# Kernel tuning notes

Hardware: AMD Instinct MI355X
Metric: run time of the kernel (lower is better)

The kernel has to match this reference:

```python
import jax, jax.numpy as jnp
import numpy as np

N, L, C, H, W, HEAD = 16, 256, 512, 32, 32, 16

def setup_inputs() -> dict:
    key = jax.random.key(0)
    ks = jax.random.split(key, 8)
    s = 0.02  # weight init scale
    return {
        "feature": jax.random.normal(ks[0], (N, C, H, W), jnp.float32),
        "token": jax.random.normal(ks[1], (N, L, C), jnp.float32),
        "wq": jax.random.normal(ks[2], (C, C), jnp.float32) * s,
        "bq": jax.random.normal(ks[3], (C,), jnp.float32) * s,
        "wk": jax.random.normal(ks[4], (C, C), jnp.float32) * s,
        "bk": jax.random.normal(ks[5], (C,), jnp.float32) * s,
        "wv": jax.random.normal(ks[6], (C, C), jnp.float32) * s,
        "bv": jax.random.normal(ks[7], (C,), jnp.float32) * s,
    }

def reference(feature, token, wq, bq, wk, bk, wv, bv):
    n, c, hgt, wid = feature.shape
    h = HEAD
    d = c // h
    l = token.shape[1]
    scale = jnp.asarray(np.sqrt(c / h), feature.dtype)
    tok = token.transpose(0, 2, 1)  # (N, C, L)
    # 1x1 conv projections == per-position GEMMs
    v = (jnp.einsum('ncl,dc->ndl', tok, wv) + bv[None, :, None]).reshape(n, h, d, l)
    k = (jnp.einsum('ncl,dc->ndl', tok, wk) + bk[None, :, None]).reshape(n, h, d, l)
    q = (jnp.einsum('nchw,dc->ndhw', feature, wq) + bq[None, :, None, None])
    q = q.reshape(n, h, d, hgt * wid).transpose(0, 1, 3, 2)  # (N, h, HW, d)
    scores = jnp.einsum('nhqd,nhdl->nhql', q, k) / scale  # (N, h, HW, L)
    coef = jax.nn.softmax(scores, axis=-1)
    proj = jnp.einsum('nhdl,nhql->nhdq', v, coef)  # (N, h, d, HW)
    return feature + proj.reshape(n, c, hgt, wid)
```

## Files before the change

### kernel.cpp

```cpp
#include <hip/hip_runtime.h>
#include <hip/hip_bf16.h>

#define N_ 16
#define L_ 256
#define C_ 512
#define HW_ 1024
#define HEADS_ 16
#define DH_ 32

typedef unsigned short u16;
typedef unsigned int u32;
typedef __attribute__((ext_vector_type(8))) short short8_t;
typedef __attribute__((ext_vector_type(4))) float f32x4;
typedef __attribute__((ext_vector_type(2))) unsigned int u32x2;

__device__ __forceinline__ u16 f2bs(float f) {
    union { float f; u32 i; } x; x.f = f;
    u32 r = x.i + 0x7fffu + ((x.i >> 16) & 1u);
    return (u16)(r >> 16);
}
__device__ __forceinline__ u32 cvt_pk_bf16(float lo, float hi) {
    u32 r;
    asm("v_cvt_pk_bf16_f32 %0, %1, %2" : "=v"(r) : "v"(lo), "v"(hi));
    return r;
}

__global__ __launch_bounds__(256) void prep_kernel(
    const float* __restrict__ token, const float* __restrict__ wq,
    const float* __restrict__ wk, const float* __restrict__ wv,
    u16* __restrict__ tokb, u16* __restrict__ wqb,
    u16* __restrict__ wkb, u16* __restrict__ wvb)
{
    const int idx = blockIdx.x * 256 + threadIdx.x;
    const float* s; u16* d; int off;
    if (idx < 524288)            { s = token; d = tokb; off = idx; }
    else if (idx < 524288+65536) { s = wq; d = wqb; off = idx - 524288; }
    else if (idx < 524288+131072){ s = wk; d = wkb; off = idx - 524288 - 65536; }
    else                         { s = wv; d = wvb; off = idx - 524288 - 131072; }
    float4 v = ((const float4*)s)[off];
    ushort4 w;
    w.x = f2bs(v.x); w.y = f2bs(v.y); w.z = f2bs(v.z); w.w = f2bs(v.w);
    ((ushort4*)d)[off] = w;
}

__global__ __launch_bounds__(256) void gemm_qf_kernel(
    const float* __restrict__ feature, const u16* __restrict__ Wb,
    const float* __restrict__ bias, u16* __restrict__ Out)
{
    __shared__ __align__(16) unsigned char smem[16384];
    u16* As = (u16*)smem;
    u16* Bs = (u16*)(smem + 8192);

    const int t = threadIdx.x;
    const int m0 = blockIdx.x * 64, n0 = blockIdx.y * 64;
    const int n = m0 >> 10, pos0 = m0 & (HW_ - 1);
    const int lane = t & 63, wid = t >> 6;
    const int i16 = lane & 15, g = lane >> 4;
    const int wm = wid >> 1, wn = wid & 1;
    const int row_a = t >> 3, c8 = t & 7;
    const int cst = t >> 2, pq = t & 3;

    f32x4 acc[2][2] = {{{0.f,0.f,0.f,0.f},{0.f,0.f,0.f,0.f}},
                       {{0.f,0.f,0.f,0.f},{0.f,0.f,0.f,0.f}}};

    for (int c0 = 0; c0 < C_; c0 += 64) {
        __syncthreads();
        #pragma unroll
        for (int r = 0; r < 2; ++r) {
            const int m = row_a + r * 32;
            *(short8_t*)&As[m * 64 + ((c8 ^ (m & 7)) << 3)] =
                *(const short8_t*)&Wb[(size_t)(n0 + m) * C_ + c0 + c8 * 8];
        }
        #pragma unroll
        for (int j = 0; j < 4; ++j) {
            const int pos = j * 16 + pq * 4;
            float4 v = *(const float4*)&feature[
                ((size_t)n * C_ + c0 + cst) * HW_ + pos0 + pos];
            ushort4 w;
            w.x = f2bs(v.x); w.y = f2bs(v.y); w.z = f2bs(v.z); w.w = f2bs(v.w);
            *(ushort4*)&Bs[(cst >> 2) * 256 + j * 64 + (cst & 3) * 16 + pq * 4] = w;
        }
        __syncthreads();
        #pragma unroll
        for (int ks = 0; ks < 2; ++ks) {
            short8_t a[2];
            #pragma unroll
            for (int mt = 0; mt < 2; ++mt) {
                const int m = wm * 32 + mt * 16 + i16;
                a[mt] = *(const short8_t*)&As[m * 64 + ((((ks << 2) | g) ^ (m & 7)) << 3)];
            }
            short8_t b[2];
            #pragma unroll
            for (int nt = 0; nt < 2; ++nt) {
                const int pb = wn * 2 + nt;
                const u32 vaddr = 8192 +
                    (u32)(ks * 32 + g * 8 + pb) * 128 + (u32)i16 * 2;
                u32x2 lo, hi;
                asm volatile("ds_read_b64_tr_b16 %0, %1"
                             : "=v"(lo) : "v"(vaddr));
                asm volatile("ds_read_b64_tr_b16 %0, %1 offset:512"
                             : "=v"(hi) : "v"(vaddr));
                union { u32 w[4]; short8_t v; } pk;
                pk.w[0] = lo[0]; pk.w[1] = lo[1];
                pk.w[2] = hi[0]; pk.w[3] = hi[1];
                b[nt] = pk.v;
            }
            asm volatile("s_waitcnt lgkmcnt(0)" ::: "memory");
            __builtin_amdgcn_sched_barrier(0);
            #pragma unroll
            for (int mt = 0; mt < 2; ++mt)
                #pragma unroll
                for (int nt = 0; nt < 2; ++nt)
                    acc[mt][nt] = __builtin_amdgcn_mfma_f32_16x16x32_bf16(
                        a[mt], b[nt], acc[mt][nt], 0, 0, 0);
        }
    }
    #pragma unroll
    for (int mt = 0; mt < 2; ++mt) {
        const int dbase = wm * 32 + mt * 16 + g * 4;
        float4 b4 = *(const float4*)&bias[n0 + dbase];
        const float bb[4] = {b4.x, b4.y, b4.z, b4.w};
        #pragma unroll
        for (int nt = 0; nt < 2; ++nt) {
            const int pos = wn * 32 + nt * 16 + i16;
            ushort4 w;
            w.x = f2bs(acc[mt][nt][0] + bb[0]);
            w.y = f2bs(acc[mt][nt][1] + bb[1]);
            w.z = f2bs(acc[mt][nt][2] + bb[2]);
            w.w = f2bs(acc[mt][nt][3] + bb[3]);
            *(ushort4*)&Out[(size_t)(m0 + pos) * C_ + n0 + dbase] = w;
        }
    }
}

__global__ __launch_bounds__(256) void gemm_kv_kernel(
    const u16* __restrict__ A, const u16* __restrict__ Wkb,
    const u16* __restrict__ Wvb, const float* __restrict__ bk,
    const float* __restrict__ bv, u16* __restrict__ Kout, u16* __restrict__ Vt)
{
    __shared__ __align__(16) unsigned char smem[24576];
    u16* As  = (u16*)smem;
    u16* Bks = (u16*)(smem + 8192);
    u16* Bvs = (u16*)(smem + 16384);
    u16 (*LTo)[72] = (u16(*)[72])smem;

    const int t = threadIdx.x;
    const int m0 = blockIdx.x * 64, n0 = blockIdx.y * 64;
    const int lane = t & 63, wid = t >> 6;
    const int i16 = lane & 15, g = lane >> 4;
    const int wm = wid >> 1, wn = wid & 1;
    const int row_a = t >> 3, c8 = t & 7;

    f32x4 ak[2][2] = {{{0.f,0.f,0.f,0.f},{0.f,0.f,0.f,0.f}},
                      {{0.f,0.f,0.f,0.f},{0.f,0.f,0.f,0.f}}};
    f32x4 av[2][2] = {{{0.f,0.f,0.f,0.f},{0.f,0.f,0.f,0.f}},
                      {{0.f,0.f,0.f,0.f},{0.f,0.f,0.f,0.f}}};
    const float bk0 = bk[n0 + wn * 32 + i16];
    const float bk1 = bk[n0 + wn * 32 + 16 + i16];
    const float bv0 = bv[n0 + wn * 32 + i16];
    const float bv1 = bv[n0 + wn * 32 + 16 + i16];

    for (int c0 = 0; c0 < C_; c0 += 64) {
        __syncthreads();
        #pragma unroll
        for (int r = 0; r < 2; ++r) {
            const int m = row_a + r * 32;
            const int sw = m * 64 + ((c8 ^ (m & 7)) << 3);
            *(short8_t*)&As[sw]  = *(const short8_t*)&A[(size_t)(m0 + m) * C_ + c0 + c8 * 8];
            *(short8_t*)&Bks[sw] = *(const short8_t*)&Wkb[(size_t)(n0 + m) * C_ + c0 + c8 * 8];
            *(short8_t*)&Bvs[sw] = *(const short8_t*)&Wvb[(size_t)(n0 + m) * C_ + c0 + c8 * 8];
        }
        __syncthreads();
        #pragma unroll
        for (int ks = 0; ks < 2; ++ks) {
            short8_t a[2], bbk[2], bbv[2];
            #pragma unroll
            for (int mt = 0; mt < 2; ++mt) {
                const int m = wm * 32 + mt * 16 + i16;
                a[mt] = *(const short8_t*)&As[m * 64 + ((((ks << 2) | g) ^ (m & 7)) << 3)];
            }
            #pragma unroll
            for (int nt = 0; nt < 2; ++nt) {
                const int d = wn * 32 + nt * 16 + i16;
                const int sw = d * 64 + ((((ks << 2) | g) ^ (d & 7)) << 3);
                bbk[nt] = *(const short8_t*)&Bks[sw];
                bbv[nt] = *(const short8_t*)&Bvs[sw];
            }
            #pragma unroll
            for (int mt = 0; mt < 2; ++mt)
                #pragma unroll
                for (int nt = 0; nt < 2; ++nt) {
                    ak[mt][nt] = __builtin_amdgcn_mfma_f32_16x16x32_bf16(
                        a[mt], bbk[nt], ak[mt][nt], 0, 0, 0);
                    av[mt][nt] = __builtin_amdgcn_mfma_f32_16x16x32_bf16(
                        a[mt], bbv[nt], av[mt][nt], 0, 0, 0);
                }
        }
    }
    const int nb = m0 >> 8, l0 = m0 & 255;
    const size_t vtbase = (size_t)nb * C_ * L_;
    #pragma unroll
    for (int mt = 0; mt < 2; ++mt)
        #pragma unroll
        for (int nt = 0; nt < 2; ++nt) {
            const int d = n0 + wn * 32 + nt * 16 + i16;
            const float bb = nt ? bv1 : bv0;
            ushort4 w;
            w.x = f2bs(av[mt][nt][0] + bb);
            w.y = f2bs(av[mt][nt][1] + bb);
            w.z = f2bs(av[mt][nt][2] + bb);
            w.w = f2bs(av[mt][nt][3] + bb);
            const int l = l0 + wm * 32 + mt * 16 + g * 4;
            *(ushort4*)&Vt[vtbase + (size_t)d * L_ + l] = w;
        }
    __syncthreads();
    #pragma unroll
    for (int mt = 0; mt < 2; ++mt)
        #pragma unroll
        for (int nt = 0; nt < 2; ++nt) {
            const float bb = nt ? bk1 : bk0;
            #pragma unroll
            for (int r = 0; r < 4; ++r)
                LTo[wm * 32 + mt * 16 + g * 4 + r][wn * 32 + nt * 16 + i16] =
                    f2bs(ak[mt][nt][r] + bb);
        }
    __syncthreads();
    #pragma unroll
    for (int rep = 0; rep < 2; ++rep) {
        const int m = (t >> 3) + rep * 32;
        const int cs = (t & 7) * 8;
        *(short8_t*)&Kout[(size_t)(m0 + m) * C_ + n0 + cs] = *(short8_t*)&LTo[m][cs];
    }
}

__global__ __launch_bounds__(256) void attn_kernel(
    const u16* __restrict__ Qws, const u16* __restrict__ Kws,
    const u16* __restrict__ Vws, const float* __restrict__ feature,
    float* __restrict__ out)
{
    __shared__ __align__(16) unsigned char smem[32768];

    const int t = threadIdx.x;
    const int wid = t >> 6, lane = t & 63;
    const int i16 = lane & 15, g = lane >> 4;
    const int pt = blockIdx.x, h = blockIdx.y, n = blockIdx.z;
    const int pos0 = pt * 64;
    const size_t qbase = ((size_t)n * HW_ + pos0) * C_ + h * DH_;
    const size_t kbase = ((size_t)n * L_) * C_ + h * DH_;
    const size_t vbase = (size_t)n * C_ * L_ + (size_t)h * DH_ * L_;

    const int q = wid * 16 + i16;

    short8_t bq = *(const short8_t*)&Qws[qbase + (size_t)q * C_ + g * 8];

    #pragma unroll
    for (int p = 0; p < 4; ++p) {
        const int kr = wid * 64 + p * 16 + (lane >> 2);
        const int kg = (lane & 3) ^ ((lane >> 3) & 3);
        const u16* ksrc = Kws + kbase + (size_t)kr * C_ + kg * 8;
        __builtin_amdgcn_global_load_lds(
            (const __attribute__((address_space(1))) void*)ksrc,
            (__attribute__((address_space(3))) void*)(smem + wid * 4096 + p * 1024),
            16, 0, 0);
        const int vd = wid * 8 + p * 2 + (lane >> 5);
        const u16* vsrc = Vws + vbase + (size_t)vd * L_ + ((lane & 31) ^ (vd & 7)) * 8;
        __builtin_amdgcn_global_load_lds(
            (const __attribute__((address_space(1))) void*)vsrc,
            (__attribute__((address_space(3))) void*)(smem + 16384 + wid * 4096 + p * 1024),
            16, 0, 0);
    }
    __syncthreads();

    const int kgr = g ^ ((i16 >> 1) & 3);
    f32x4 s[16];
    #pragma unroll
    for (int nf = 0; nf < 16; ++nf) {
        short8_t a = *(const short8_t*)(smem + (nf * 16 + i16) * 64 + kgr * 16);
        f32x4 z = {0.f, 0.f, 0.f, 0.f};
        s[nf] = __builtin_amdgcn_mfma_f32_16x16x32_bf16(a, bq, z, 0, 0, 0);
    }

    float mm[16], sm[16];
    #pragma unroll
    for (int nf = 0; nf < 16; ++nf)
        mm[nf] = fmaxf(fmaxf(s[nf][0], s[nf][1]), fmaxf(s[nf][2], s[nf][3]));
    #pragma unroll
    for (int st = 8; st >= 1; st >>= 1)
        #pragma unroll
        for (int i = 0; i < 8; ++i)
            if (i < st) mm[i] = fmaxf(mm[i], mm[i + st]);
    float m = mm[0];
    m = fmaxf(m, __shfl_xor(m, 16));
    m = fmaxf(m, __shfl_xor(m, 32));

    const float K2 = 0.25506288f;
    #pragma unroll
    for (int nf = 0; nf < 16; ++nf) {
        #pragma unroll
        for (int r = 0; r < 4; ++r) s[nf][r] = exp2f((s[nf][r] - m) * K2);
        sm[nf] = (s[nf][0] + s[nf][1]) + (s[nf][2] + s[nf][3]);
    }
    #pragma unroll
    for (int st = 8; st >= 1; st >>= 1)
        #pragma unroll
        for (int i = 0; i < 8; ++i)
            if (i < st) sm[i] += sm[i + st];
    float ssum = sm[0];
    ssum += __shfl_xor(ssum, 16);
    ssum += __shfl_xor(ssum, 32);
    const float pinv = 1.0f / ssum;

    __syncthreads();

    f32x4 o0 = {0.f, 0.f, 0.f, 0.f}, o1 = {0.f, 0.f, 0.f, 0.f};
    const int e7 = i16 & 7;

    #pragma unroll
    for (int hb = 0; hb < 2; ++hb) {
        #pragma unroll
        for (int nfp = 0; nfp < 8; ++nfp) {
            const int nf = hb * 8 + nfp;
            #pragma unroll
            for (int w = 0; w < 2; ++w) {
                u32 pw = cvt_pk_bf16(s[nf][2 * w] * pinv, s[nf][2 * w + 1] * pinv);
                const int gran = (nfp * 2 + (g >> 1)) ^ e7;
                *(u32*)(smem + q * 256 + gran * 16 + ((g & 1) * 2 + w) * 4) = pw;
            }
        }
        __syncthreads();
        #pragma unroll
        for (int ks = 0; ks < 4; ++ks) {
            short8_t pb = *(const short8_t*)(smem + q * 256 + (((ks * 4 + g) ^ e7) * 16));
            const int vg = (((hb * 4 + ks) * 4 + g) ^ e7) * 16;
            short8_t va0 = *(const short8_t*)(smem + 16384 + i16 * 512 + vg);
            short8_t va1 = *(const short8_t*)(smem + 16384 + (16 + i16) * 512 + vg);
            o0 = __builtin_amdgcn_mfma_f32_16x16x32_bf16(va0, pb, o0, 0, 0, 0);
            o1 = __builtin_amdgcn_mfma_f32_16x16x32_bf16(va1, pb, o1, 0, 0, 0);
        }
        if (hb == 0) __syncthreads();
    }

    const size_t obase = ((size_t)n * C_ + h * DH_) * HW_ + pos0 + q;
    #pragma unroll
    for (int r = 0; r < 4; ++r) {
        const size_t oa = obase + (size_t)(g * 4 + r) * HW_;
        out[oa] = feature[oa] + o0[r];
        const size_t ob = obase + (size_t)(16 + g * 4 + r) * HW_;
        out[ob] = feature[ob] + o1[r];
    }
}

extern "C" void kernel_launch(void* const* d_in, const int* in_sizes, int n_in,
                              void* d_out, int out_size, void* d_ws, size_t ws_size,
                              hipStream_t stream)
{
    const float* feature = (const float*)d_in[0];
    const float* token   = (const float*)d_in[1];
    const float* wq      = (const float*)d_in[2];
    const float* bq      = (const float*)d_in[3];
    const float* wk      = (const float*)d_in[4];
    const float* bk      = (const float*)d_in[5];
    const float* wv      = (const float*)d_in[6];
    const float* bv      = (const float*)d_in[7];
    float* out = (float*)d_out;

    u16* Qws = (u16*)d_ws;
    u16* Kws = Qws + (size_t)N_ * HW_ * C_;
    u16* Vws = Kws + (size_t)N_ * L_ * C_;

    char* ob = (char*)d_out;
    u16* tokb = (u16*)(ob + (16u << 20));
    u16* wqb  = (u16*)(ob + (20u << 20));
    u16* wkb  = (u16*)(ob + (20u << 20) + 524288);
    u16* wvb  = (u16*)(ob + (20u << 20) + 1048576);

    prep_kernel<<<dim3(2816), 256, 0, stream>>>(token, wq, wk, wv,
                                                tokb, wqb, wkb, wvb);
    gemm_qf_kernel<<<dim3(256, 8), 256, 0, stream>>>(feature, wqb, bq, Qws);
    gemm_kv_kernel<<<dim3(64, 8), 256, 0, stream>>>(tokb, wkb, wvb, bk, bv,
                                                    Kws, Vws);
    attn_kernel<<<dim3(16, 16, 16), 256, 0, stream>>>(Qws, Kws, Vws, feature, out);
}
```

Baseline: 78.96 us.

## Fuse bf16 prep and Q/KV projection GEMMs into one proj kernel

Drops the separate fp32-to-bf16 prep kernel and the two projection GEMM launches, replacing them with one kernel whose blocks split into a K/V branch and a Q branch. Each branch converts fp32 token and weight tiles to bf16 inline while staging them into shared memory. The Q branch also reorders the feature tile load and preloads both k-steps of fragments before the MFMAs. This removes two launches and the intermediate bf16 round trip through global memory, at the cost of converting the weights again in every block and running a larger, divergent kernel.

```diff
diff --git a/kernel.cpp b/kernel.cpp
--- a/kernel.cpp
+++ b/kernel.cpp
@@ -24,212 +24,205 @@
     asm("v_cvt_pk_bf16_f32 %0, %1, %2" : "=v"(r) : "v"(lo), "v"(hi));
     return r;
 }
-
-__global__ __launch_bounds__(256) void prep_kernel(
-    const float* __restrict__ token, const float* __restrict__ wq,
-    const float* __restrict__ wk, const float* __restrict__ wv,
-    u16* __restrict__ tokb, u16* __restrict__ wqb,
-    u16* __restrict__ wkb, u16* __restrict__ wvb)
+__device__ __forceinline__ void cvt8(const float* __restrict__ src, void* dst) {
+    float4 lo = *(const float4*)src;
+    float4 hi = *(const float4*)(src + 4);
+    union { u32 w[4]; short8_t v; } pk;
+    pk.w[0] = cvt_pk_bf16(lo.x, lo.y);
+    pk.w[1] = cvt_pk_bf16(lo.z, lo.w);
+    pk.w[2] = cvt_pk_bf16(hi.x, hi.y);
+    pk.w[3] = cvt_pk_bf16(hi.z, hi.w);
+    *(short8_t*)dst = pk.v;
+}
+
+__global__ __launch_bounds__(256) void proj_kernel(
+    const float* __restrict__ feature, const float* __restrict__ token,
+    const float* __restrict__ wq, const float* __restrict__ bq,
+    const float* __restrict__ wk, const float* __restrict__ bk,
+    const float* __restrict__ wv, const float* __restrict__ bv,
+    u16* __restrict__ Qout, u16* __restrict__ Kout, u16* __restrict__ Vt)
 {
-    const int idx = blockIdx.x * 256 + threadIdx.x;
-    const float* s; u16* d; int off;
-    if (idx < 524288)            { s = token; d = tokb; off = idx; }
-    else if (idx < 524288+65536) { s = wq; d = wqb; off = idx - 524288; }
-    else if (idx < 524288+131072){ s = wk; d = wkb; off = idx - 524288 - 65536; }
-    else                         { s = wv; d = wvb; off = idx - 524288 - 131072; }
-    float4 v = ((const float4*)s)[off];
-    ushort4 w;
-    w.x = f2bs(v.x); w.y = f2bs(v.y); w.z = f2bs(v.z); w.w = f2bs(v.w);
-    ((ushort4*)d)[off] = w;
-}
-
-__global__ __launch_bounds__(256) void gemm_qf_kernel(
-    const float* __restrict__ feature, const u16* __restrict__ Wb,
-    const float* __restrict__ bias, u16* __restrict__ Out)
-{
-    __shared__ __align__(16) unsigned char smem[16384];
-    u16* As = (u16*)smem;
-    u16* Bs = (u16*)(smem + 8192);
+    __shared__ __align__(16) unsigned char smem[24576];
 
     const int t = threadIdx.x;
-    const int m0 = blockIdx.x * 64, n0 = blockIdx.y * 64;
-    const int n = m0 >> 10, pos0 = m0 & (HW_ - 1);
     const int lane = t & 63, wid = t >> 6;
     const int i16 = lane & 15, g = lane >> 4;
     const int wm = wid >> 1, wn = wid & 1;
-    const int row_a = t >> 3, c8 = t & 7;
-    const int cst = t >> 2, pq = t & 3;
-
-    f32x4 acc[2][2] = {{{0.f,0.f,0.f,0.f},{0.f,0.f,0.f,0.f}},
-                       {{0.f,0.f,0.f,0.f},{0.f,0.f,0.f,0.f}}};
-
-    for (int c0 = 0; c0 < C_; c0 += 64) {
+
+    if (blockIdx.x < 512) {
+        u16* As  = (u16*)smem;
+        u16* Bks = (u16*)(smem + 8192);
+        u16* Bvs = (u16*)(smem + 16384);
+        u16 (*LTo)[72] = (u16(*)[72])smem;
+
+        const int m0 = (blockIdx.x & 63) * 64, n0 = (blockIdx.x >> 6) * 64;
+        const int row_a = t >> 3, c8 = t & 7;
+
+        f32x4 ak[2][2] = {{{0.f,0.f,0.f,0.f},{0.f,0.f,0.f,0.f}},
+                          {{0.f,0.f,0.f,0.f},{0.f,0.f,0.f,0.f}}};
+        f32x4 av[2][2] = {{{0.f,0.f,0.f,0.f},{0.f,0.f,0.f,0.f}},
+                          {{0.f,0.f,0.f,0.f},{0.f,0.f,0.f,0.f}}};
+        const float bk0 = bk[n0 + wn * 32 + i16];
+        const float bk1 = bk[n0 + wn * 32 + 16 + i16];
+        const float bv0 = bv[n0 + wn * 32 + i16];
+        const float bv1 = bv[n0 + wn * 32 + 16 + i16];
+
+        for (int c0 = 0; c0 < C_; c0 += 64) {
+            __syncthreads();
+            #pragma unroll
+            for (int r = 0; r < 2; ++r) {
+                const int m = row_a + r * 32;
+                const int sw = m * 64 + ((c8 ^ (m & 7)) << 3);
+                cvt8(&token[(size_t)(m0 + m) * C_ + c0 + c8 * 8], &As[sw]);
+                cvt8(&wk[(size_t)(n0 + m) * C_ + c0 + c8 * 8], &Bks[sw]);
+                cvt8(&wv[(size_t)(n0 + m) * C_ + c0 + c8 * 8], &Bvs[sw]);
+            }
+            __syncthreads();
+            #pragma unroll
+            for (int ks = 0; ks < 2; ++ks) {
+                short8_t a[2], bbk[2], bbv[2];
+                #pragma unroll
+                for (int mt = 0; mt < 2; ++mt) {
+                    const int m = wm * 32 + mt * 16 + i16;
+                    a[mt] = *(const short8_t*)&As[m * 64 + ((((ks << 2) | g) ^ (m & 7)) << 3)];
+                }
+                #pragma unroll
+                for (int nt = 0; nt < 2; ++nt) {
+                    const int d = wn * 32 + nt * 16 + i16;
+                    const int sw = d * 64 + ((((ks << 2) | g) ^ (d & 7)) << 3);
+                    bbk[nt] = *(const short8_t*)&Bks[sw];
+                    bbv[nt] = *(const short8_t*)&Bvs[sw];
+                }
+                #pragma unroll
+                for (int mt = 0; mt < 2; ++mt)
+                    #pragma unroll
+                    for (int nt = 0; nt < 2; ++nt) {
+                        ak[mt][nt] = __builtin_amdgcn_mfma_f32_16x16x32_bf16(
+                            a[mt], bbk[nt], ak[mt][nt], 0, 0, 0);
+                        av[mt][nt] = __builtin_amdgcn_mfma_f32_16x16x32_bf16(
+                            a[mt], bbv[nt], av[mt][nt], 0, 0, 0);
+                    }
+            }
+        }
+        const int nb = m0 >> 8, l0 = m0 & 255;
+        const size_t vtbase = (size_t)nb * C_ * L_;
+        #pragma unroll
+        for (int mt = 0; mt < 2; ++mt)
+            #pragma unroll
+            for (int nt = 0; nt < 2; ++nt) {
+                const int d = n0 + wn * 32 + nt * 16 + i16;
+                const float bb = nt ? bv1 : bv0;
+                ushort4 w;
+                w.x = f2bs(av[mt][nt][0] + bb);
+                w.y = f2bs(av[mt][nt][1] + bb);
+                w.z = f2bs(av[mt][nt][2] + bb);
+                w.w = f2bs(av[mt][nt][3] + bb);
+                const int l = l0 + wm * 32 + mt * 16 + g * 4;
+                *(ushort4*)&Vt[vtbase + (size_t)d * L_ + l] = w;
+            }
         __syncthreads();
         #pragma unroll
-        for (int r = 0; r < 2; ++r) {
-            const int m = row_a + r * 32;
-            *(short8_t*)&As[m * 64 + ((c8 ^ (m & 7)) << 3)] =
-                *(const short8_t*)&Wb[(size_t)(n0 + m) * C_ + c0 + c8 * 8];
-        }
-        #pragma unroll
-        for (int j = 0; j < 4; ++j) {
-            const int pos = j * 16 + pq * 4;
-            float4 v = *(const float4*)&feature[
-                ((size_t)n * C_ + c0 + cst) * HW_ + pos0 + pos];
-            ushort4 w;
-            w.x = f2bs(v.x); w.y = f2bs(v.y); w.z = f2bs(v.z); w.w = f2bs(v.w);
-            *(ushort4*)&Bs[(cst >> 2) * 256 + j * 64 + (cst & 3) * 16 + pq * 4] = w;
-        }
+        for (int mt = 0; mt < 2; ++mt)
+            #pragma unroll
+            for (int nt = 0; nt < 2; ++nt) {
+                const float bb = nt ? bk1 : bk0;
+                #pragma unroll
+                for (int r = 0; r < 4; ++r)
+                    LTo[wm * 32 + mt * 16 + g * 4 + r][wn * 32 + nt * 16 + i16] =
+                        f2bs(ak[mt][nt][r] + bb);
+            }
         __syncthreads();
         #pragma unroll
-        for (int ks = 0; ks < 2; ++ks) {
-            short8_t a[2];
-            #pragma unroll
-            for (int mt = 0; mt < 2; ++mt) {
-                const int m = wm * 32 + mt * 16 + i16;
-                a[mt] = *(const short8_t*)&As[m * 64 + ((((ks << 2) | g) ^ (m & 7)) << 3)];
-            }
-            short8_t b[2];
-            #pragma unroll
-            for (int nt = 0; nt < 2; ++nt) {
-                const int pb = wn * 2 + nt;
-                const u32 vaddr = 8192 +
-                    (u32)(ks * 32 + g * 8 + pb) * 128 + (u32)i16 * 2;
-                u32x2 lo, hi;
-                asm volatile("ds_read_b64_tr_b16 %0, %1"
-                             : "=v"(lo) : "v"(vaddr));
-                asm volatile("ds_read_b64_tr_b16 %0, %1 offset:512"
-                             : "=v"(hi) : "v"(vaddr));
-                union { u32 w[4]; short8_t v; } pk;
-                pk.w[0] = lo[0]; pk.w[1] = lo[1];
-                pk.w[2] = hi[0]; pk.w[3] = hi[1];
-                b[nt] = pk.v;
-            }
+        for (int rep = 0; rep < 2; ++rep) {
+            const int m = (t >> 3) + rep * 32;
+            const int cs = (t & 7) * 8;
+            *(short8_t*)&Kout[(size_t)(m0 + m) * C_ + n0 + cs] = *(short8_t*)&LTo[m][cs];
+        }
+    } else {
+        u16* As = (u16*)smem;
+        u16* Bs = (u16*)(smem + 8192);
+
+        const int bid = blockIdx.x - 512;
+        const int m0 = (bid & 255) * 64, n0 = (bid >> 8) * 64;
+        const int n = m0 >> 10, pos0 = m0 & (HW_ - 1);
+        const int row_a = t >> 3, c8 = t & 7;
+
+        f32x4 acc[2][2] = {{{0.f,0.f,0.f,0.f},{0.f,0.f,0.f,0.f}},
+                           {{0.f,0.f,0.f,0.f},{0.f,0.f,0.f,0.f}}};
+
+        for (int c0 = 0; c0 < C_; c0 += 64) {
+            __syncthreads();
+            #pragma unroll
+            for (int r = 0; r < 2; ++r) {
+                const int m = row_a + r * 32;
+                cvt8(&wq[(size_t)(n0 + m) * C_ + c0 + c8 * 8],
+                     &As[m * 64 + ((c8 ^ (m & 7)) << 3)]);
+            }
+            #pragma unroll
+            for (int ps = 0; ps < 4; ++ps) {
+                const int row = ps * 16 + (t >> 4);
+                const int px = (t & 15) * 4;
+                float4 v = *(const float4*)&feature[
+                    ((size_t)n * C_ + c0 + row) * HW_ + pos0 + px];
+                ushort4 w;
+                w.x = f2bs(v.x); w.y = f2bs(v.y);
+                w.z = f2bs(v.z); w.w = f2bs(v.w);
+                *(ushort4*)&Bs[(row >> 2) * 256 + (px >> 4) * 64 +
+                               (row & 3) * 16 + (px & 15)] = w;
+            }
+            __syncthreads();
+            short8_t a2[2][2], b2[2][2];
+            #pragma unroll
+            for (int ks = 0; ks < 2; ++ks)
+                #pragma unroll
+                for (int mt = 0; mt < 2; ++mt) {
+                    const int m = wm * 32 + mt * 16 + i16;
+                    a2[ks][mt] = *(const short8_t*)&As[m * 64 + ((((ks << 2) | g) ^ (m & 7)) << 3)];
+                }
+            #pragma unroll
+            for (int ks = 0; ks < 2; ++ks)
+                #pragma unroll
+                for (int nt = 0; nt < 2; ++nt) {
+                    const int pb = wn * 2 + nt;
+                    const u32 vaddr = 8192 +
+                        (u32)(ks * 32 + g * 8 + pb) * 128 + (u32)i16 * 2;
+                    u32x2 lo, hi;
+                    asm volatile("ds_read_b64_tr_b16 %0, %1"
+                                 : "=v"(lo) : "v"(vaddr));
+                    asm volatile("ds_read_b64_tr_b16 %0, %1 offset:512"
+                                 : "=v"(hi) : "v"(vaddr));
+                    union { u32 w[4]; short8_t v; } pk;
+                    pk.w[0] = lo[0]; pk.w[1] = lo[1];
+                    pk.w[2] = hi[0]; pk.w[3] = hi[1];
+                    b2[ks][nt] = pk.v;
+                }
             asm volatile("s_waitcnt lgkmcnt(0)" ::: "memory");
             __builtin_amdgcn_sched_barrier(0);
             #pragma unroll
-            for (int mt = 0; mt < 2; ++mt)
-                #pragma unroll
-                for (int nt = 0; nt < 2; ++nt)
-                    acc[mt][nt] = __builtin_amdgcn_mfma_f32_16x16x32_bf16(
-                        a[mt], b[nt], acc[mt][nt], 0, 0, 0);
-        }
-    }
-    #pragma unroll
-    for (int mt = 0; mt < 2; ++mt) {
-        const int dbase = wm * 32 + mt * 16 + g * 4;
-        float4 b4 = *(const float4*)&bias[n0 + dbase];
-        const float bb[4] = {b4.x, b4.y, b4.z, b4.w};
-        #pragma unroll
-        for (int nt = 0; nt < 2; ++nt) {
-            const int pos = wn * 32 + nt * 16 + i16;
-            ushort4 w;
-            w.x = f2bs(acc[mt][nt][0] + bb[0]);
-            w.y = f2bs(acc[mt][nt][1] + bb[1]);
-            w.z = f2bs(acc[mt][nt][2] + bb[2]);
-            w.w = f2bs(acc[mt][nt][3] + bb[3]);
-            *(ushort4*)&Out[(size_t)(m0 + pos) * C_ + n0 + dbase] = w;
-        }
-    }
-}
-
-__global__ __launch_bounds__(256) void gemm_kv_kernel(
-    const u16* __restrict__ A, const u16* __restrict__ Wkb,
-    const u16* __restrict__ Wvb, const float* __restrict__ bk,
-    const float* __restrict__ bv, u16* __restrict__ Kout, u16* __restrict__ Vt)
-{
-    __shared__ __align__(16) unsigned char smem[24576];
-    u16* As  = (u16*)smem;
-    u16* Bks = (u16*)(smem + 8192);
-    u16* Bvs = (u16*)(smem + 16384);
-    u16 (*LTo)[72] = (u16(*)[72])smem;
-
-    const int t = threadIdx.x;
-    const int m0 = blockIdx.x * 64, n0 = blockIdx.y * 64;
-    const int lane = t & 63, wid = t >> 6;
-    const int i16 = lane & 15, g = lane >> 4;
-    const int wm = wid >> 1, wn = wid & 1;
-    const int row_a = t >> 3, c8 = t & 7;
-
-    f32x4 ak[2][2] = {{{0.f,0.f,0.f,0.f},{0.f,0.f,0.f,0.f}},
-                      {{0.f,0.f,0.f,0.f},{0.f,0.f,0.f,0.f}}};
-    f32x4 av[2][2] = {{{0.f,0.f,0.f,0.f},{0.f,0.f,0.f,0.f}},
-                      {{0.f,0.f,0.f,0.f},{0.f,0.f,0.f,0.f}}};
-    const float bk0 = bk[n0 + wn * 32 + i16];
-    const float bk1 = bk[n0 + wn * 32 + 16 + i16];
-    const float bv0 = bv[n0 + wn * 32 + i16];
-    const float bv1 = bv[n0 + wn * 32 + 16 + i16];
-
-    for (int c0 = 0; c0 < C_; c0 += 64) {
-        __syncthreads();
-        #pragma unroll
-        for (int r = 0; r < 2; ++r) {
-            const int m = row_a + r * 32;
-            const int sw = m * 64 + ((c8 ^ (m & 7)) << 3);
-            *(short8_t*)&As[sw]  = *(const short8_t*)&A[(size_t)(m0 + m) * C_ + c0 + c8 * 8];
-            *(short8_t*)&Bks[sw] = *(const short8_t*)&Wkb[(size_t)(n0 + m) * C_ + c0 + c8 * 8];
-            *(short8_t*)&Bvs[sw] = *(const short8_t*)&Wvb[(size_t)(n0 + m) * C_ + c0 + c8 * 8];
-        }
-        __syncthreads();
-        #pragma unroll
-        for (int ks = 0; ks < 2; ++ks) {
-            short8_t a[2], bbk[2], bbv[2];
-            #pragma unroll
-            for (int mt = 0; mt < 2; ++mt) {
-                const int m = wm * 32 + mt * 16 + i16;
-                a[mt] = *(const short8_t*)&As[m * 64 + ((((ks << 2) | g) ^ (m & 7)) << 3)];
-            }
+            for (int ks = 0; ks < 2; ++ks)
+                #pragma unroll
+                for (int mt = 0; mt < 2; ++mt)
+                    #pragma unroll
+                    for (int nt = 0; nt < 2; ++nt)
+                        acc[mt][nt] = __builtin_amdgcn_mfma_f32_16x16x32_bf16(
+                            a2[ks][mt], b2[ks][nt], acc[mt][nt], 0, 0, 0);
+        }
+        #pragma unroll
+        for (int mt = 0; mt < 2; ++mt) {
+            const int dbase = wm * 32 + mt * 16 + g * 4;
+            float4 b4 = *(const float4*)&bq[n0 + dbase];
+            const float bb[4] = {b4.x, b4.y, b4.z, b4.w};
             #pragma unroll
             for (int nt = 0; nt < 2; ++nt) {
-                const int d = wn * 32 + nt * 16 + i16;
-                const int sw = d * 64 + ((((ks << 2) | g) ^ (d & 7)) << 3);
-                bbk[nt] = *(const short8_t*)&Bks[sw];
-                bbv[nt] = *(const short8_t*)&Bvs[sw];
-            }
-            #pragma unroll
-            for (int mt = 0; mt < 2; ++mt)
-                #pragma unroll
-                for (int nt = 0; nt < 2; ++nt) {
-                    ak[mt][nt] = __builtin_amdgcn_mfma_f32_16x16x32_bf16(
-                        a[mt], bbk[nt], ak[mt][nt], 0, 0, 0);
-                    av[mt][nt] = __builtin_amdgcn_mfma_f32_16x16x32_bf16(
-                        a[mt], bbv[nt], av[mt][nt], 0, 0, 0);
-                }
-        }
-    }
-    const int nb = m0 >> 8, l0 = m0 & 255;
-    const size_t vtbase = (size_t)nb * C_ * L_;
-    #pragma unroll
-    for (int mt = 0; mt < 2; ++mt)
-        #pragma unroll
-        for (int nt = 0; nt < 2; ++nt) {
-            const int d = n0 + wn * 32 + nt * 16 + i16;
-            const float bb = nt ? bv1 : bv0;
-            ushort4 w;
-            w.x = f2bs(av[mt][nt][0] + bb);
-            w.y = f2bs(av[mt][nt][1] + bb);
-            w.z = f2bs(av[mt][nt][2] + bb);
-            w.w = f2bs(av[mt][nt][3] + bb);
-            const int l = l0 + wm * 32 + mt * 16 + g * 4;
-            *(ushort4*)&Vt[vtbase + (size_t)d * L_ + l] = w;
-        }
-    __syncthreads();
-    #pragma unroll
-    for (int mt = 0; mt < 2; ++mt)
-        #pragma unroll
-        for (int nt = 0; nt < 2; ++nt) {
-            const float bb = nt ? bk1 : bk0;
-            #pragma unroll
-            for (int r = 0; r < 4; ++r)
-                LTo[wm * 32 + mt * 16 + g * 4 + r][wn * 32 + nt * 16 + i16] =
-                    f2bs(ak[mt][nt][r] + bb);
-        }
-    __syncthreads();
-    #pragma unroll
-    for (int rep = 0; rep < 2; ++rep) {
-        const int m = (t >> 3) + rep * 32;
-        const int cs = (t & 7) * 8;
-        *(short8_t*)&Kout[(size_t)(m0 + m) * C_ + n0 + cs] = *(short8_t*)&LTo[m][cs];
+                const int pos = wn * 32 + nt * 16 + i16;
+                ushort4 w;
+                w.x = f2bs(acc[mt][nt][0] + bb[0]);
+                w.y = f2bs(acc[mt][nt][1] + bb[1]);
+                w.z = f2bs(acc[mt][nt][2] + bb[2]);
+                w.w = f2bs(acc[mt][nt][3] + bb[3]);
+                *(ushort4*)&Qout[(size_t)(m0 + pos) * C_ + n0 + dbase] = w;
+            }
+        }
     }
 }
 
@@ -255,8 +248,8 @@
 
     #pragma unroll
     for (int p = 0; p < 4; ++p) {
+        const int kg = (lane & 3) ^ ((lane >> 3) & 3);
         const int kr = wid * 64 + p * 16 + (lane >> 2);
-        const int kg = (lane & 3) ^ ((lane >> 3) & 3);
         const u16* ksrc = Kws + kbase + (size_t)kr * C_ + kg * 8;
         __builtin_amdgcn_global_load_lds(
             (const __attribute__((address_space(1))) void*)ksrc,
@@ -368,16 +361,8 @@
     u16* Kws = Qws + (size_t)N_ * HW_ * C_;
     u16* Vws = Kws + (size_t)N_ * L_ * C_;
 
-    char* ob = (char*)d_out;
-    u16* tokb = (u16*)(ob + (16u << 20));
-    u16* wqb  = (u16*)(ob + (20u << 20));
-    u16* wkb  = (u16*)(ob + (20u << 20) + 524288);
-    u16* wvb  = (u16*)(ob + (20u << 20) + 1048576);
-
-    prep_kernel<<<dim3(2816), 256, 0, stream>>>(token, wq, wk, wv,
-                                                tokb, wqb, wkb, wvb);
-    gemm_qf_kernel<<<dim3(256, 8), 256, 0, stream>>>(feature, wqb, bq, Qws);
-    gemm_kv_kernel<<<dim3(64, 8), 256, 0, stream>>>(tokb, wkb, wvb, bk, bv,
-                                                    Kws, Vws);
+    proj_kernel<<<dim3(2560), 256, 0, stream>>>(feature, token, wq, bq,
+                                                wk, bk, wv, bv,
+                                                Qws, Kws, Vws);
     attn_kernel<<<dim3(16, 16, 16), 256, 0, stream>>>(Qws, Kws, Vws, feature, out);
 }
```

New measurement: 79.37 us. About the same (+0.5%).

## Merge Q and KV projection GEMMs into one launch with larger tiles

Applied to the files above, without the earlier changes.

Combines the separate Q-projection and K/V-projection GEMM kernels into a single proj_kernel. Blocks below 256 compute K/V and the rest compute Q, which removes a launch and lets both GEMMs share the GPU at once. Tiles grow to 128x64 for KV and 128x128 for Q, operand tiles are loaded with global_load_lds direct-to-LDS copies, and block indices are remapped so consecutive tiles stay on the same XCD. The larger tiles raise register and LDS use (36 KB), which may lower occupancy, and the mixed block roles can leave the load unbalanced.

```diff
diff --git a/kernel.cpp b/kernel.cpp
--- a/kernel.cpp
+++ b/kernel.cpp
@@ -24,6 +24,18 @@
     asm("v_cvt_pk_bf16_f32 %0, %1, %2" : "=v"(r) : "v"(lo), "v"(hi));
     return r;
 }
+__device__ __forceinline__ void cvt8(const float* __restrict__ src, void* dst) {
+    float4 lo = *(const float4*)src;
+    float4 hi = *(const float4*)(src + 4);
+    union { u32 w[4]; short8_t v; } pk;
+    pk.w[0] = cvt_pk_bf16(lo.x, lo.y);
+    pk.w[1] = cvt_pk_bf16(lo.z, lo.w);
+    pk.w[2] = cvt_pk_bf16(hi.x, hi.y);
+    pk.w[3] = cvt_pk_bf16(hi.z, hi.w);
+    *(short8_t*)dst = pk.v;
+}
+#define AS1(p) (const __attribute__((address_space(1))) void*)(p)
+#define AS3(p) (__attribute__((address_space(3))) void*)(p)
 
 __global__ __launch_bounds__(256) void prep_kernel(
     const float* __restrict__ token, const float* __restrict__ wq,
@@ -43,193 +55,215 @@
     ((ushort4*)d)[off] = w;
 }
 
-__global__ __launch_bounds__(256) void gemm_qf_kernel(
-    const float* __restrict__ feature, const u16* __restrict__ Wb,
-    const float* __restrict__ bias, u16* __restrict__ Out)
+__global__ __launch_bounds__(256) void proj_kernel(
+    const float* __restrict__ feature,
+    const u16* __restrict__ tokb, const u16* __restrict__ wqb,
+    const u16* __restrict__ wkb, const u16* __restrict__ wvb,
+    const float* __restrict__ bq, const float* __restrict__ bk,
+    const float* __restrict__ bv,
+    u16* __restrict__ Qout, u16* __restrict__ Kout, u16* __restrict__ Vt)
 {
-    __shared__ __align__(16) unsigned char smem[16384];
-    u16* As = (u16*)smem;
-    u16* Bs = (u16*)(smem + 8192);
+    __shared__ __align__(16) unsigned char smem[36864];
 
     const int t = threadIdx.x;
-    const int m0 = blockIdx.x * 64, n0 = blockIdx.y * 64;
-    const int n = m0 >> 10, pos0 = m0 & (HW_ - 1);
     const int lane = t & 63, wid = t >> 6;
     const int i16 = lane & 15, g = lane >> 4;
-    const int wm = wid >> 1, wn = wid & 1;
-    const int row_a = t >> 3, c8 = t & 7;
-    const int cst = t >> 2, pq = t & 3;
-
-    f32x4 acc[2][2] = {{{0.f,0.f,0.f,0.f},{0.f,0.f,0.f,0.f}},
-                       {{0.f,0.f,0.f,0.f},{0.f,0.f,0.f,0.f}}};
-
-    for (int c0 = 0; c0 < C_; c0 += 64) {
-        __syncthreads();
-        #pragma unroll
-        for (int r = 0; r < 2; ++r) {
-            const int m = row_a + r * 32;
-            *(short8_t*)&As[m * 64 + ((c8 ^ (m & 7)) << 3)] =
-                *(const short8_t*)&Wb[(size_t)(n0 + m) * C_ + c0 + c8 * 8];
-        }
-        #pragma unroll
-        for (int j = 0; j < 4; ++j) {
-            const int pos = j * 16 + pq * 4;
-            float4 v = *(const float4*)&feature[
-                ((size_t)n * C_ + c0 + cst) * HW_ + pos0 + pos];
-            ushort4 w;
-            w.x = f2bs(v.x); w.y = f2bs(v.y); w.z = f2bs(v.z); w.w = f2bs(v.w);
-            *(ushort4*)&Bs[(cst >> 2) * 256 + j * 64 + (cst & 3) * 16 + pq * 4] = w;
-        }
-        __syncthreads();
-        #pragma unroll
-        for (int ks = 0; ks < 2; ++ks) {
-            short8_t a[2];
-            #pragma unroll
-            for (int mt = 0; mt < 2; ++mt) {
-                const int m = wm * 32 + mt * 16 + i16;
-                a[mt] = *(const short8_t*)&As[m * 64 + ((((ks << 2) | g) ^ (m & 7)) << 3)];
-            }
-            short8_t b[2];
+
+    if (blockIdx.x < 256) {
+        const int xcd = blockIdx.x & 7, j = blockIdx.x >> 3;
+        const int m0 = (xcd * 4 + (j & 3)) * 128;
+        const int n0 = (j >> 2) * 64;
+        u16* Tok = (u16*)smem;
+        u16* Bk  = (u16*)(smem + 16384);
+        u16* Bv  = (u16*)(smem + 24576);
+        u16 (*LTo)[72] = (u16(*)[72])smem;
+
+        const int wm = wid >> 1, wn = wid & 1;
+        const int r8 = t >> 3, gr = t & 7;
+
+        f32x4 ak[4][2], av[4][2];
+        #pragma unroll
+        for (int mt = 0; mt < 4; ++mt)
             #pragma unroll
             for (int nt = 0; nt < 2; ++nt) {
-                const int pb = wn * 2 + nt;
-                const u32 vaddr = 8192 +
-                    (u32)(ks * 32 + g * 8 + pb) * 128 + (u32)i16 * 2;
-                u32x2 lo, hi;
-                asm volatile("ds_read_b64_tr_b16 %0, %1"
-                             : "=v"(lo) : "v"(vaddr));
-                asm volatile("ds_read_b64_tr_b16 %0, %1 offset:512"
-                             : "=v"(hi) : "v"(vaddr));
-                union { u32 w[4]; short8_t v; } pk;
-                pk.w[0] = lo[0]; pk.w[1] = lo[1];
-                pk.w[2] = hi[0]; pk.w[3] = hi[1];
-                b[nt] = pk.v;
-            }
-            asm volatile("s_waitcnt lgkmcnt(0)" ::: "memory");
-            __builtin_amdgcn_sched_barrier(0);
-            #pragma unroll
-            for (int mt = 0; mt < 2; ++mt)
-                #pragma unroll
-                for (int nt = 0; nt < 2; ++nt)
-                    acc[mt][nt] = __builtin_amdgcn_mfma_f32_16x16x32_bf16(
-                        a[mt], b[nt], acc[mt][nt], 0, 0, 0);
-        }
-    }
-    #pragma unroll
-    for (int mt = 0; mt < 2; ++mt) {
-        const int dbase = wm * 32 + mt * 16 + g * 4;
-        float4 b4 = *(const float4*)&bias[n0 + dbase];
-        const float bb[4] = {b4.x, b4.y, b4.z, b4.w};
-        #pragma unroll
-        for (int nt = 0; nt < 2; ++nt) {
-            const int pos = wn * 32 + nt * 16 + i16;
-            ushort4 w;
-            w.x = f2bs(acc[mt][nt][0] + bb[0]);
-            w.y = f2bs(acc[mt][nt][1] + bb[1]);
-            w.z = f2bs(acc[mt][nt][2] + bb[2]);
-            w.w = f2bs(acc[mt][nt][3] + bb[3]);
-            *(ushort4*)&Out[(size_t)(m0 + pos) * C_ + n0 + dbase] = w;
-        }
-    }
-}
-
-__global__ __launch_bounds__(256) void gemm_kv_kernel(
-    const u16* __restrict__ A, const u16* __restrict__ Wkb,
-    const u16* __restrict__ Wvb, const float* __restrict__ bk,
-    const float* __restrict__ bv, u16* __restrict__ Kout, u16* __restrict__ Vt)
-{
-    __shared__ __align__(16) unsigned char smem[24576];
-    u16* As  = (u16*)smem;
-    u16* Bks = (u16*)(smem + 8192);
-    u16* Bvs = (u16*)(smem + 16384);
-    u16 (*LTo)[72] = (u16(*)[72])smem;
-
-    const int t = threadIdx.x;
-    const int m0 = blockIdx.x * 64, n0 = blockIdx.y * 64;
-    const int lane = t & 63, wid = t >> 6;
-    const int i16 = lane & 15, g = lane >> 4;
-    const int wm = wid >> 1, wn = wid & 1;
-    const int row_a = t >> 3, c8 = t & 7;
-
-    f32x4 ak[2][2] = {{{0.f,0.f,0.f,0.f},{0.f,0.f,0.f,0.f}},
-                      {{0.f,0.f,0.f,0.f},{0.f,0.f,0.f,0.f}}};
-    f32x4 av[2][2] = {{{0.f,0.f,0.f,0.f},{0.f,0.f,0.f,0.f}},
-                      {{0.f,0.f,0.f,0.f},{0.f,0.f,0.f,0.f}}};
-    const float bk0 = bk[n0 + wn * 32 + i16];
-    const float bk1 = bk[n0 + wn * 32 + 16 + i16];
-    const float bv0 = bv[n0 + wn * 32 + i16];
-    const float bv1 = bv[n0 + wn * 32 + 16 + i16];
-
-    for (int c0 = 0; c0 < C_; c0 += 64) {
-        __syncthreads();
-        #pragma unroll
-        for (int r = 0; r < 2; ++r) {
-            const int m = row_a + r * 32;
-            const int sw = m * 64 + ((c8 ^ (m & 7)) << 3);
-            *(short8_t*)&As[sw]  = *(const short8_t*)&A[(size_t)(m0 + m) * C_ + c0 + c8 * 8];
-            *(short8_t*)&Bks[sw] = *(const short8_t*)&Wkb[(size_t)(n0 + m) * C_ + c0 + c8 * 8];
-            *(short8_t*)&Bvs[sw] = *(const short8_t*)&Wvb[(size_t)(n0 + m) * C_ + c0 + c8 * 8];
-        }
-        __syncthreads();
-        #pragma unroll
-        for (int ks = 0; ks < 2; ++ks) {
-            short8_t a[2], bbk[2], bbv[2];
-            #pragma unroll
-            for (int mt = 0; mt < 2; ++mt) {
-                const int m = wm * 32 + mt * 16 + i16;
-                a[mt] = *(const short8_t*)&As[m * 64 + ((((ks << 2) | g) ^ (m & 7)) << 3)];
-            }
-            #pragma unroll
-            for (int nt = 0; nt < 2; ++nt) {
-                const int d = wn * 32 + nt * 16 + i16;
-                const int sw = d * 64 + ((((ks << 2) | g) ^ (d & 7)) << 3);
-                bbk[nt] = *(const short8_t*)&Bks[sw];
-                bbv[nt] = *(const short8_t*)&Bvs[sw];
-            }
-            #pragma unroll
-            for (int mt = 0; mt < 2; ++mt)
+                ak[mt][nt] = (f32x4){0.f, 0.f, 0.f, 0.f};
+                av[mt][nt] = (f32x4){0.f, 0.f, 0.f, 0.f};
+            }
+
+        for (int c0 = 0; c0 < C_; c0 += 64) {
+            __syncthreads();
+            #pragma unroll
+            for (int p = 0; p < 4; ++p) {
+                const int row = p * 32 + r8;
+                __builtin_amdgcn_global_load_lds(
+                    AS1(tokb + (size_t)(m0 + row) * C_ + c0 + ((gr ^ (row & 7)) << 3)),
+                    AS3(smem + (p * 32 + wid * 8) * 128), 16, 0, 0);
+            }
+            #pragma unroll
+            for (int p = 0; p < 2; ++p) {
+                const int row = p * 32 + r8;
+                const int gs = (gr ^ (row & 7)) << 3;
+                __builtin_amdgcn_global_load_lds(
+                    AS1(wkb + (size_t)(n0 + row) * C_ + c0 + gs),
+                    AS3(smem + 16384 + (p * 32 + wid * 8) * 128), 16, 0, 0);
+                __builtin_amdgcn_global_load_lds(
+                    AS1(wvb + (size_t)(n0 + row) * C_ + c0 + gs),
+                    AS3(smem + 24576 + (p * 32 + wid * 8) * 128), 16, 0, 0);
+            }
+            __syncthreads();
+            #pragma unroll
+            for (int ks = 0; ks < 2; ++ks) {
+                short8_t a[4], bbk[2], bbv[2];
+                #pragma unroll
+                for (int mt = 0; mt < 4; ++mt) {
+                    const int m = wm * 64 + mt * 16 + i16;
+                    a[mt] = *(const short8_t*)&Tok[m * 64 + ((((ks << 2) | g) ^ (m & 7)) << 3)];
+                }
                 #pragma unroll
                 for (int nt = 0; nt < 2; ++nt) {
-                    ak[mt][nt] = __builtin_amdgcn_mfma_f32_16x16x32_bf16(
-                        a[mt], bbk[nt], ak[mt][nt], 0, 0, 0);
-                    av[mt][nt] = __builtin_amdgcn_mfma_f32_16x16x32_bf16(
-                        a[mt], bbv[nt], av[mt][nt], 0, 0, 0);
+                    const int d = wn * 32 + nt * 16 + i16;
+                    const int sw = d * 64 + ((((ks << 2) | g) ^ (d & 7)) << 3);
+                    bbk[nt] = *(const short8_t*)&Bk[sw];
+                    bbv[nt] = *(const short8_t*)&Bv[sw];
                 }
-        }
-    }
-    const int nb = m0 >> 8, l0 = m0 & 255;
-    const size_t vtbase = (size_t)nb * C_ * L_;
-    #pragma unroll
-    for (int mt = 0; mt < 2; ++mt)
+                #pragma unroll
+                for (int mt = 0; mt < 4; ++mt)
+                    #pragma unroll
+                    for (int nt = 0; nt < 2; ++nt) {
+                        ak[mt][nt] = __builtin_amdgcn_mfma_f32_16x16x32_bf16(
+                            a[mt], bbk[nt], ak[mt][nt], 0, 0, 0);
+                        av[mt][nt] = __builtin_amdgcn_mfma_f32_16x16x32_bf16(
+                            a[mt], bbv[nt], av[mt][nt], 0, 0, 0);
+                    }
+            }
+        }
+        const int nb = m0 >> 8, l0 = m0 & 255;
+        const size_t vtbase = (size_t)nb * C_ * L_;
         #pragma unroll
         for (int nt = 0; nt < 2; ++nt) {
             const int d = n0 + wn * 32 + nt * 16 + i16;
-            const float bb = nt ? bv1 : bv0;
-            ushort4 w;
-            w.x = f2bs(av[mt][nt][0] + bb);
-            w.y = f2bs(av[mt][nt][1] + bb);
-            w.z = f2bs(av[mt][nt][2] + bb);
-            w.w = f2bs(av[mt][nt][3] + bb);
-            const int l = l0 + wm * 32 + mt * 16 + g * 4;
-            *(ushort4*)&Vt[vtbase + (size_t)d * L_ + l] = w;
-        }
-    __syncthreads();
-    #pragma unroll
-    for (int mt = 0; mt < 2; ++mt)
+            const float bb = bv[d];
+            #pragma unroll
+            for (int mt = 0; mt < 4; ++mt) {
+                ushort4 w;
+                w.x = f2bs(av[mt][nt][0] + bb);
+                w.y = f2bs(av[mt][nt][1] + bb);
+                w.z = f2bs(av[mt][nt][2] + bb);
+                w.w = f2bs(av[mt][nt][3] + bb);
+                const int l = l0 + wm * 64 + mt * 16 + g * 4;
+                *(ushort4*)&Vt[vtbase + (size_t)d * L_ + l] = w;
+            }
+        }
+        __syncthreads();
         #pragma unroll
         for (int nt = 0; nt < 2; ++nt) {
-            const float bb = nt ? bk1 : bk0;
-            #pragma unroll
-            for (int r = 0; r < 4; ++r)
-                LTo[wm * 32 + mt * 16 + g * 4 + r][wn * 32 + nt * 16 + i16] =
-                    f2bs(ak[mt][nt][r] + bb);
-        }
-    __syncthreads();
-    #pragma unroll
-    for (int rep = 0; rep < 2; ++rep) {
-        const int m = (t >> 3) + rep * 32;
-        const int cs = (t & 7) * 8;
-        *(short8_t*)&Kout[(size_t)(m0 + m) * C_ + n0 + cs] = *(short8_t*)&LTo[m][cs];
+            const int col = wn * 32 + nt * 16 + i16;
+            const float bb = bk[n0 + col];
+            #pragma unroll
+            for (int mt = 0; mt < 4; ++mt)
+                #pragma unroll
+                for (int r = 0; r < 4; ++r)
+                    LTo[wm * 64 + mt * 16 + g * 4 + r][col] =
+                        f2bs(ak[mt][nt][r] + bb);
+        }
+        __syncthreads();
+        #pragma unroll
+        for (int rep = 0; rep < 4; ++rep) {
+            const int m = (t >> 3) + rep * 32;
+            const int cs = (t & 7) * 8;
+            *(short8_t*)&Kout[(size_t)(m0 + m) * C_ + n0 + cs] = *(short8_t*)&LTo[m][cs];
+        }
+    } else {
+        const int qid = blockIdx.x - 256;
+        const int xcd = qid & 7, j = qid >> 3;
+        const int m0 = (xcd * 16 + (j & 15)) * 128;
+        const int n0 = (j >> 4) * 128;
+        const int n = m0 >> 10, pos0 = m0 & (HW_ - 1);
+        u16* Wt = (u16*)smem;
+        const int FB = 16384;
+
+        const int wq_pos = wid >> 1, wq_d = wid & 1;
+        const int r8 = t >> 3, gr = t & 7;
+
+        f32x4 acc[4][4];
+        #pragma unroll
+        for (int dm = 0; dm < 4; ++dm)
+            #pragma unroll
+            for (int pf = 0; pf < 4; ++pf)
+                acc[dm][pf] = (f32x4){0.f, 0.f, 0.f, 0.f};
+
+        for (int c0 = 0; c0 < C_; c0 += 64) {
+            __syncthreads();
+            #pragma unroll
+            for (int p = 0; p < 4; ++p) {
+                const int row = p * 32 + r8;
+                __builtin_amdgcn_global_load_lds(
+                    AS1(wqb + (size_t)(n0 + row) * C_ + c0 + ((gr ^ (row & 7)) << 3)),
+                    AS3(smem + (p * 32 + wid * 8) * 128), 16, 0, 0);
+            }
+            #pragma unroll
+            for (int p = 0; p < 4; ++p) {
+                const int row = p * 16 + (t >> 4);
+                const int pos8 = (t & 15) * 8;
+                float f8[8];
+                *(float4*)&f8[0] = *(const float4*)&feature[
+                    ((size_t)n * C_ + c0 + row) * HW_ + pos0 + pos8];
+                *(float4*)&f8[4] = *(const float4*)&feature[
+                    ((size_t)n * C_ + c0 + row) * HW_ + pos0 + pos8 + 4];
+                const int cb = row >> 2, cr = row & 3;
+                const int pb = pos8 >> 4, po = (pos8 & 15) * 2;
+                cvt8(f8, smem + FB + (cb * 8 + pb) * 160 + cr * 32 + po);
+            }
+            __syncthreads();
+            #pragma unroll
+            for (int ks = 0; ks < 2; ++ks) {
+                short8_t a[4], b[4];
+                #pragma unroll
+                for (int dm = 0; dm < 4; ++dm) {
+                    const int m = wq_d * 64 + dm * 16 + i16;
+                    a[dm] = *(const short8_t*)&Wt[m * 64 + ((((ks << 2) | g) ^ (m & 7)) << 3)];
+                }
+                #pragma unroll
+                for (int pf = 0; pf < 4; ++pf) {
+                    const int pb = wq_pos * 4 + pf;
+                    const u32 vaddr = FB +
+                        (u32)((ks * 8 + g * 2) * 8 + pb) * 160 + (u32)i16 * 2;
+                    u32x2 lo, hi;
+                    asm volatile("ds_read_b64_tr_b16 %0, %1"
+                                 : "=v"(lo) : "v"(vaddr));
+                    asm volatile("ds_read_b64_tr_b16 %0, %1 offset:1280"
+                                 : "=v"(hi) : "v"(vaddr));
+                    union { u32 w[4]; short8_t v; } pk;
+                    pk.w[0] = lo[0]; pk.w[1] = lo[1];
+                    pk.w[2] = hi[0]; pk.w[3] = hi[1];
+                    b[pf] = pk.v;
+                }
+                asm volatile("s_waitcnt lgkmcnt(0)" ::: "memory");
+                __builtin_amdgcn_sched_barrier(0);
+                #pragma unroll
+                for (int dm = 0; dm < 4; ++dm)
+                    #pragma unroll
+                    for (int pf = 0; pf < 4; ++pf)
+                        acc[dm][pf] = __builtin_amdgcn_mfma_f32_16x16x32_bf16(
+                            a[dm], b[pf], acc[dm][pf], 0, 0, 0);
+            }
+        }
+        #pragma unroll
+        for (int dm = 0; dm < 4; ++dm) {
+            const int dbase = wq_d * 64 + dm * 16 + g * 4;
+            float4 b4 = *(const float4*)&bq[n0 + dbase];
+            const float bb[4] = {b4.x, b4.y, b4.z, b4.w};
+            #pragma unroll
+            for (int pf = 0; pf < 4; ++pf) {
+                const int pos = wq_pos * 64 + pf * 16 + i16;
+                ushort4 w;
+                w.x = f2bs(acc[dm][pf][0] + bb[0]);
+                w.y = f2bs(acc[dm][pf][1] + bb[1]);
+                w.z = f2bs(acc[dm][pf][2] + bb[2]);
+                w.w = f2bs(acc[dm][pf][3] + bb[3]);
+                *(ushort4*)&Qout[(size_t)(m0 + pos) * C_ + n0 + dbase] = w;
+            }
+        }
     }
 }
 
@@ -255,19 +289,15 @@
 
     #pragma unroll
     for (int p = 0; p < 4; ++p) {
+        const int kg = (lane & 3) ^ ((lane >> 3) & 3);
         const int kr = wid * 64 + p * 16 + (lane >> 2);
-        const int kg = (lane & 3) ^ ((lane >> 3) & 3);
         const u16* ksrc = Kws + kbase + (size_t)kr * C_ + kg * 8;
-        __builtin_amdgcn_global_load_lds(
-            (const __attribute__((address_space(1))) void*)ksrc,
-            (__attribute__((address_space(3))) void*)(smem + wid * 4096 + p * 1024),
-            16, 0, 0);
+        __builtin_amdgcn_global_load_lds(AS1(ksrc),
+            AS3(smem + wid * 4096 + p * 1024), 16, 0, 0);
         const int vd = wid * 8 + p * 2 + (lane >> 5);
         const u16* vsrc = Vws + vbase + (size_t)vd * L_ + ((lane & 31) ^ (vd & 7)) * 8;
-        __builtin_amdgcn_global_load_lds(
-            (const __attribute__((address_space(1))) void*)vsrc,
-            (__attribute__((address_space(3))) void*)(smem + 16384 + wid * 4096 + p * 1024),
-            16, 0, 0);
+        __builtin_amdgcn_global_load_lds(AS1(vsrc),
+            AS3(smem + 16384 + wid * 4096 + p * 1024), 16, 0, 0);
     }
     __syncthreads();
 
@@ -376,8 +406,7 @@
 
     prep_kernel<<<dim3(2816), 256, 0, stream>>>(token, wq, wk, wv,
                                                 tokb, wqb, wkb, wvb);
-    gemm_qf_kernel<<<dim3(256, 8), 256, 0, stream>>>(feature, wqb, bq, Qws);
-    gemm_kv_kernel<<<dim3(64, 8), 256, 0, stream>>>(tokb, wkb, wvb, bk, bv,
-                                                    Kws, Vws);
+    proj_kernel<<<dim3(768), 256, 0, stream>>>(feature, tokb, wqb, wkb, wvb,
+                                               bq, bk, bv, Qws, Kws, Vws);
     attn_kernel<<<dim3(16, 16, 16), 256, 0, stream>>>(Qws, Kws, Vws, feature, out);
 }
```

New measurement: 76.32 us. -3.4%, faster.
